# Performance work log

Measured on AMD Instinct MI355X. Metric: run time of the kernel, lower is better.

Reference implementation:

```python
import jax, jax.numpy as jnp
import numpy as np
from jax import lax

B_IDX = 0  # label_vocab['B']
E_IDX = 1  # label_vocab['E']
NEG = -10000.0


def setup_inputs() -> dict:
    key = jax.random.key(0)
    k1, k2 = jax.random.split(key)
    B, T, L = 256, 512, 64
    X = jax.random.normal(k1, (B, T, L), dtype=jnp.float32)
    transition = jax.random.normal(k2, (L, L), dtype=jnp.float32)
    # __init__ masking: no transitions out of 'E', none into 'B'
    transition = transition.at[E_IDX, :].set(NEG)
    transition = transition.at[:, B_IDX].set(NEG)
    return {"X": X, "transition": transition}


def reference(X, transition):
    # CRF forward (alpha) recursion, vectorized over the tag dimension and
    # batched; recurrence over timesteps carried by lax.scan.
    B, T, L = X.shape
    init_alpha = jnp.full((B, L), NEG, dtype=X.dtype).at[:, B_IDX].set(0.0)

    def step(alpha, x_t):
        # alpha: [B, L] (prev tag), x_t: [B, L] (emission for next tag)
        # next_var[b, prev, nxt] = alpha[b, prev] + transition[prev, nxt] + x_t[b, nxt]
        next_var = alpha[:, :, None] + transition[None, :, :] + x_t[:, None, :]
        new_alpha = jax.nn.logsumexp(next_var, axis=1)  # reduce over prev tag
        return new_alpha, None

    X_tbl = jnp.moveaxis(X, 1, 0)  # [T, B, L]
    final_alpha, _ = lax.scan(step, init_alpha, X_tbl)
    return final_alpha  # [B, L]
```

## Files before the change

### kernel.cpp

```cpp
#include <hip/hip_runtime.h>

#define LTAG 64
#define NEGV -10000.0f
#define L2E 1.4426950408889634f
#define LN2 0.6931471805599453f

__device__ __forceinline__ float exp2_fast(float x) { return __builtin_amdgcn_exp2f(x); }
__device__ __forceinline__ float log2_fast(float x) { return __builtin_amdgcn_logf(x); }

__device__ __forceinline__ float readlane_f(float v, int lane) {
    return __int_as_float(__builtin_amdgcn_readlane(__float_as_int(v), lane));
}

__global__ __launch_bounds__(64) void crf_forward_kernel(
    const float* __restrict__ X, const float* __restrict__ trans,
    float* __restrict__ out, int T) {
    const int lane = threadIdx.x;
    const int b = blockIdx.x;
    const float* xb = X + (size_t)b * T * LTAG + lane;

    float etr[LTAG];
    float c2 = -3.0e38f;
#pragma unroll
    for (int p = 0; p < LTAG; ++p) {
        etr[p] = trans[p * LTAG + lane] * L2E;
        c2 = fmaxf(c2, etr[p]);
    }
#pragma unroll
    for (int p = 0; p < LTAG; ++p) etr[p] = exp2_fast(etr[p] - c2);

    float A = (lane == 0) ? 1.0f : 0.0f;
    float SH = 0.0f;
    float sB = 1.0f, xB = 0.0f, shB = 0.0f;

    float xr[4];
#pragma unroll
    for (int i = 0; i < 4; ++i) xr[i] = xb[(size_t)i * LTAG];

    for (int t = 0; t < T; t += 4) {
#pragma unroll
        for (int u = 0; u < 4; ++u) {
            const float xcur = xr[u];
            int tpf = t + u + 4;
            tpf = tpf < T ? tpf : T - 1;
            xr[u] = xb[(size_t)tpf * LTAG];

            const float g = exp2_fast(fmaf(xcur, L2E, c2));

            float ub[LTAG];
#pragma unroll
            for (int p = 0; p < LTAG; ++p) ub[p] = readlane_f(A, p);

            float s0 = 0.f, s1 = 0.f, s2 = 0.f, s3 = 0.f;
#pragma unroll
            for (int p = 0; p < LTAG; p += 4) {
                s0 = fmaf(ub[p + 0], etr[p + 0], s0);
                s1 = fmaf(ub[p + 1], etr[p + 1], s1);
                s2 = fmaf(ub[p + 2], etr[p + 2], s2);
                s3 = fmaf(ub[p + 3], etr[p + 3], s3);
            }
            const float s = (s0 + s1) + (s2 + s3);

            sB = s; xB = xcur; shB = SH;
            A = s * g;

            if (u == 3) {
                float mm = fmaxf(readlane_f(A, 2), readlane_f(A, 19));
                mm = fmaxf(mm, readlane_f(A, 28));
                mm = fmaxf(mm, fmaxf(readlane_f(A, 37), readlane_f(A, 53)));
                int eb2 = (__float_as_int(mm) >> 23) & 0xff;
                eb2 = eb2 < 1 ? 1 : eb2;
                A *= __int_as_float((254 - eb2) << 23);
                SH += (float)(eb2 - 127);
            }
        }
    }

    float res;
    if (lane == 0) {
        res = (log2_fast(sB) + fmaf(xB, L2E, c2) + shB) * LN2;
    } else {
        res = (log2_fast(A) + SH) * LN2;
    }
    out[b * LTAG + lane] = res;
}

extern "C" void kernel_launch(void* const* d_in, const int* in_sizes, int n_in,
                              void* d_out, int out_size, void* d_ws, size_t ws_size,
                              hipStream_t stream) {
    const float* X = (const float*)d_in[0];
    const float* trans = (const float*)d_in[1];
    float* out = (float*)d_out;

    const int B = out_size / LTAG;
    const int T = in_sizes[0] / (B * LTAG);

    crf_forward_kernel<<<B, LTAG, 0, stream>>>(X, trans, out, T);
}
```

Measured before the change: 180.5 us.

## Replace readlane broadcast matvec with diagonal bpermute rotation scheme

Swaps the 64 scalar readlane broadcasts per step for 31 ds_bpermute rotations plus one half-wave swap. Each lane accumulates over diagonals, using transition weights stored in skewed order. The second half of the diagonals is folded in through the xor-32 partner lane. This cuts the per-step broadcast count and removes SGPR serialization, but it moves the exchange onto the LDS crossbar, whose latency may lengthen the serial dependency chain.

```diff
diff --git a/kernel.cpp b/kernel.cpp
--- a/kernel.cpp
+++ b/kernel.cpp
@@ -1,7 +1,6 @@
 #include <hip/hip_runtime.h>
 
 #define LTAG 64
-#define NEGV -10000.0f
 #define L2E 1.4426950408889634f
 #define LN2 0.6931471805599453f
 
@@ -11,6 +10,9 @@
 __device__ __forceinline__ float readlane_f(float v, int lane) {
     return __int_as_float(__builtin_amdgcn_readlane(__float_as_int(v), lane));
 }
+__device__ __forceinline__ float bperm_f(int abytes, float v) {
+    return __int_as_float(__builtin_amdgcn_ds_bpermute(abytes, __float_as_int(v)));
+}
 
 __global__ __launch_bounds__(64) void crf_forward_kernel(
     const float* __restrict__ X, const float* __restrict__ trans,
@@ -19,15 +21,28 @@
     const int b = blockIdx.x;
     const float* xb = X + (size_t)b * T * LTAG + lane;
 
-    float etr[LTAG];
+    const int swaddr = (lane ^ 32) << 2;
+
+    float er[32], w[32];
     float c2 = -3.0e38f;
+    {
+        float tmp[64];
 #pragma unroll
-    for (int p = 0; p < LTAG; ++p) {
-        etr[p] = trans[p * LTAG + lane] * L2E;
-        c2 = fmaxf(c2, etr[p]);
+        for (int d = 0; d < 64; ++d) {
+            tmp[d] = trans[(((lane + d) & 63) << 6) + lane] * L2E;
+            c2 = fmaxf(c2, tmp[d]);
+        }
+#pragma unroll
+        for (int d = 0; d < 64; ++d) tmp[d] = exp2_fast(tmp[d] - c2);
+#pragma unroll
+        for (int d = 0; d < 32; ++d) er[d] = tmp[d];
+#pragma unroll
+        for (int d = 0; d < 32; ++d) w[d] = bperm_f(swaddr, tmp[d + 32]);
     }
+
+    int adr[32];
 #pragma unroll
-    for (int p = 0; p < LTAG; ++p) etr[p] = exp2_fast(etr[p] - c2);
+    for (int d = 0; d < 32; ++d) adr[d] = ((lane + d) & 63) << 2;
 
     float A = (lane == 0) ? 1.0f : 0.0f;
     float SH = 0.0f;
@@ -47,19 +62,24 @@
 
             const float g = exp2_fast(fmaf(xcur, L2E, c2));
 
-            float ub[LTAG];
+            float s0 = A * er[0];
+            float u0 = A * w[0];
+            float s1 = 0.f, u1 = 0.f;
 #pragma unroll
-            for (int p = 0; p < LTAG; ++p) ub[p] = readlane_f(A, p);
-
-            float s0 = 0.f, s1 = 0.f, s2 = 0.f, s3 = 0.f;
-#pragma unroll
-            for (int p = 0; p < LTAG; p += 4) {
-                s0 = fmaf(ub[p + 0], etr[p + 0], s0);
-                s1 = fmaf(ub[p + 1], etr[p + 1], s1);
-                s2 = fmaf(ub[p + 2], etr[p + 2], s2);
-                s3 = fmaf(ub[p + 3], etr[p + 3], s3);
+            for (int d = 1; d < 32; ++d) {
+                const float r = bperm_f(adr[d], A);
+                if (d & 1) {
+                    s1 = fmaf(r, er[d], s1);
+                    u1 = fmaf(r, w[d], u1);
+                } else {
+                    s0 = fmaf(r, er[d], s0);
+                    u0 = fmaf(r, w[d], u0);
+                }
             }
-            const float s = (s0 + s1) + (s2 + s3);
+            const float slo = s0 + s1;
+            const float uu = u0 + u1;
+            const float shi = bperm_f(swaddr, uu);
+            const float s = slo + shi;
 
             sB = s; xB = xcur; shB = SH;
             A = s * g;
```

After: 216.5 us. +19.9%, slower.
